# Kernel optimization log

Measured on AMD Instinct MI355X. Metric: run time of the kernel, lower is better.

The kernel has to match this reference:

```python
import jax, jax.numpy as jnp
import numpy as np

# Faithful RBF layer math:
# dists[n,k] = sum_d relu(sigma[d]) * (x[n,d]-center[k,d])^2  (original builds an NxN
# matrix per center just to take its diagonal; we use the algebraic expansion
# x^2.s - 2 (x*s).c^T + c^2.s which is O(N*K*D) and identical math)
# D2 = 1 - dists * relu(width); concat bias column of ones; out = D2_bias @ relu(W_out)

N, D, K, OUT = 131072, 256, 256, 128

def setup_inputs() -> dict:
    key = jax.random.key(0)
    k1, k2, k3, k4 = jax.random.split(key, 4)
    x = jax.random.normal(k1, (N, D), dtype=jnp.float32)
    # 'uniform' keras initializer ~ U(-0.05, 0.05)
    center = jax.random.uniform(k2, (K, D), minval=-0.05, maxval=0.05, dtype=jnp.float32)
    sigma = jax.random.uniform(k3, (1, D), minval=0.5, maxval=1.0, dtype=jnp.float32)
    width = jnp.ones((1, K), dtype=jnp.float32)
    output_weights = jax.random.uniform(k4, (1 + K, OUT), minval=0.5, maxval=1.0, dtype=jnp.float32)
    return {"x": x, "center": center, "sigma": sigma, "width": width,
            "output_weights": output_weights}

def reference(x, center, sigma, width, output_weights):
    s = jax.nn.relu(sigma[0])                       # [D]
    x2 = (x * x) @ s                                # [N]
    c2 = (center * center) @ s                      # [K]
    cross = (x * s) @ center.T                      # [N,K]
    dists = x2[:, None] - 2.0 * cross + c2[None, :] # [N,K] weighted sq-dists
    D2 = 1.0 - dists * jax.nn.relu(width)           # [N,K]
    ones = jnp.ones((x.shape[0], 1), dtype=x.dtype)
    D2_bias = jnp.concatenate([ones, D2], axis=1)   # [N,1+K]
    return D2_bias @ jax.nn.relu(output_weights)    # [N,OUT]
```

## Files before the change

### kernel.cpp

```cpp
#include <hip/hip_runtime.h>


typedef short  short8 __attribute__((ext_vector_type(8)));
typedef __bf16 bf16x8 __attribute__((ext_vector_type(8)));
typedef float  f32x4  __attribute__((ext_vector_type(4)));

#define N_ 131072
#define D_ 256
#define K_ 256
#define O_ 128

__device__ __forceinline__ unsigned short f2bf_bits(float f) {
  unsigned u = __builtin_bit_cast(unsigned, f);
  u += 0x7fffu + ((u >> 16) & 1u);
  return (unsigned short)(u >> 16);
}

__device__ __forceinline__ float relu(float v) { return v > 0.f ? v : 0.f; }

__global__ __launch_bounds__(256) void rbf_pre(
    const float* __restrict__ center, const float* __restrict__ sigma,
    const float* __restrict__ width,  const float* __restrict__ W,
    short* __restrict__ Mfrag, float* __restrict__ Bo, float* __restrict__ S1)
{
  const int tid = threadIdx.x;
  if (blockIdx.x < 64) {
    const int ot = blockIdx.x & 7;
    const int ks = blockIdx.x >> 3;
    __shared__ float ww[K_][16];
    __shared__ float cen[K_][32];
#pragma unroll
    for (int i = 0; i < 16; ++i) {
      const int k  = i * 16 + (tid >> 4);
      const int oc = tid & 15;
      ww[k][oc] = relu(width[k]) * relu(W[(1 + k) * O_ + ot * 16 + oc]);
    }
#pragma unroll
    for (int i = 0; i < 32; ++i) {
      const int k  = i * 8 + (tid >> 5);
      const int dc = tid & 31;
      cen[k][dc] = center[k * D_ + ks * 32 + dc];
    }
    __syncthreads();
    const int j   = tid & 7;
    const int lf  = tid >> 3;
    const int oc  = lf & 15;
    const int dc1 = (lf >> 4) * 8 + j;
    float a1 = 0.f, a2 = 0.f;
#pragma unroll 8
    for (int k = 0; k < K_; ++k) {
      const float w = ww[k][oc];
      a1 = fmaf(cen[k][dc1],      w, a1);
      a2 = fmaf(cen[k][dc1 + 16], w, a2);
    }
    const int e1 = blockIdx.x * 512 + tid;
    const int d1 = ks * 32 + dc1;
    Mfrag[e1]       = (short)f2bf_bits(a1 * relu(sigma[d1]));
    Mfrag[e1 + 256] = (short)f2bf_bits(a2 * relu(sigma[d1 + 16]));
  } else {
    __shared__ float c2s[K_];
    {
      const f32x4* cr = (const f32x4*)(center + tid * D_);
      const f32x4* sr = (const f32x4*)sigma;
      f32x4 acc = {0.f, 0.f, 0.f, 0.f};
#pragma unroll 8
      for (int d4 = 0; d4 < D_ / 4; ++d4) {
        const f32x4 c = cr[d4];
        const f32x4 s = sr[d4];
#pragma unroll
        for (int e = 0; e < 4; ++e) acc[e] = fmaf(c[e] * c[e], relu(s[e]), acc[e]);
      }
      c2s[tid] = (acc[0] + acc[1]) + (acc[2] + acc[3]);
    }
    __syncthreads();
    if (tid < O_) {
      const int o = tid;
      float s1 = 0.f, sum = 0.f, c2w = 0.f;
#pragma unroll 4
      for (int k = 0; k < K_; ++k) {
        const float w  = relu(width[k]);
        const float wr = relu(W[(1 + k) * O_ + o]);
        s1  = fmaf(w, wr, s1);
        sum += wr;
        c2w = fmaf(c2s[k] * w, wr, c2w);
      }
      Bo[o] = relu(W[o]) + sum - c2w;
      S1[o] = s1;
    }
  }
}

__global__ __launch_bounds__(512, 2) void rbf_main(
    const float* __restrict__ x, const float* __restrict__ sigma,
    const short* __restrict__ Mfrag, const float* __restrict__ Bo,
    const float* __restrict__ S1, float* __restrict__ out)
{
  __shared__ short8 Blds[4096];
  const int tid  = threadIdx.x;
  const int lane = tid & 63;
  const int wv   = tid >> 6;
  const int m    = lane & 15;
  const int q    = lane >> 4;
  const long rowBase = ((long)blockIdx.x * 8 + wv) * 16;

  short8 stg[8];
  const short8* Mf8 = (const short8*)Mfrag;
#pragma unroll
  for (int i = 0; i < 8; ++i) stg[i] = Mf8[i * 512 + tid];

  const float* xr = x + (rowBase + m) * D_ + q * 8;
  f32x4 raw[16];
#pragma unroll
  for (int ks = 0; ks < 8; ++ks) {
    raw[2 * ks]     = *(const f32x4*)(xr + ks * 32);
    raw[2 * ks + 1] = *(const f32x4*)(xr + ks * 32 + 4);
  }

#pragma unroll
  for (int i = 0; i < 8; ++i) Blds[i * 512 + tid] = stg[i];

  const float* sp = sigma + q * 8;
  bf16x8 a[8];
  float x2 = 0.f;
#pragma unroll
  for (int ks = 0; ks < 8; ++ks) {
    float sv[8], v[8];
    *(f32x4*)(sv)     = *(const f32x4*)(sp + ks * 32);
    *(f32x4*)(sv + 4) = *(const f32x4*)(sp + ks * 32 + 4);
    *(f32x4*)(v)      = raw[2 * ks];
    *(f32x4*)(v + 4)  = raw[2 * ks + 1];
    short8 ab;
#pragma unroll
    for (int jj = 0; jj < 8; ++jj) {
      const float s = relu(sv[jj]);
      x2 = fmaf(s * v[jj], v[jj], x2);
      ab[jj] = (short)f2bf_bits(v[jj]);
    }
    a[ks] = __builtin_bit_cast(bf16x8, ab);
  }
  x2 += __shfl_xor(x2, 16);
  x2 += __shfl_xor(x2, 32);

  __syncthreads();

#pragma unroll
  for (int ot = 0; ot < 8; ++ot) {
    f32x4 acc = {0.f, 0.f, 0.f, 0.f};
#pragma unroll
    for (int ks = 0; ks < 8; ++ks) {
      const bf16x8 bb =
          __builtin_bit_cast(bf16x8, Blds[(ks * 8 + ot) * 64 + lane]);
      acc = __builtin_amdgcn_mfma_f32_16x16x32_bf16(a[ks], bb, acc, 0, 0, 0);
    }
    const int   o  = ot * 16 + m;
    const float bo = Bo[o];
    const float s1 = S1[o];
    float* op = out + rowBase * O_ + o;
#pragma unroll
    for (int r = 0; r < 4; ++r) {
      const int rr = q * 4 + r;
      const float x2r = __shfl(x2, rr);
      op[(long)rr * O_] = fmaf(2.f, acc[r], fmaf(-x2r, s1, bo));
    }
  }
}

extern "C" void kernel_launch(void* const* d_in, const int* in_sizes, int n_in,
                              void* d_out, int out_size, void* d_ws, size_t ws_size,
                              hipStream_t stream) {
  (void)in_sizes; (void)n_in; (void)out_size; (void)ws_size;
  const float* x      = (const float*)d_in[0];
  const float* center = (const float*)d_in[1];
  const float* sigma  = (const float*)d_in[2];
  const float* width  = (const float*)d_in[3];
  const float* W      = (const float*)d_in[4];
  float* out = (float*)d_out;

  short* Mfrag = (short*)d_ws;
  float* Bo    = (float*)((char*)d_ws + 65536);
  float* S1    = (float*)((char*)d_ws + 66048);

  hipLaunchKernelGGL(rbf_pre, dim3(65), dim3(256), 0, stream,
                     center, sigma, width, W, Mfrag, Bo, S1);
  hipLaunchKernelGGL(rbf_main, dim3(1024), dim3(512), 0, stream,
                     x, sigma, Mfrag, Bo, S1, out);
}
```

Baseline: 249.3 us.

## Permute output columns for vectorized stores, async LDS load, higher occupancy

Permutes the output-column order inside the precomputed weight fragments so each lane owns four contiguous output columns. This lets the epilogue write with 16-byte vector stores instead of scalar strided stores. The B-fragment staging now uses global_load_lds to copy straight into LDS, bypassing registers. The MFMA loop is reordered to keep all eight accumulators live, the bias/S1 loads are hoisted and vectorized, and launch bounds are raised to four blocks per SM, which risks register pressure with eight accumulators plus the A fragments.

```diff
diff --git a/kernel.cpp b/kernel.cpp
--- a/kernel.cpp
+++ b/kernel.cpp
@@ -29,11 +29,12 @@
     const int ks = blockIdx.x >> 3;
     __shared__ float ww[K_][16];
     __shared__ float cen[K_][32];
+    const int ocol = (ot >> 2) * 64 + (tid & 15) * 4 + (ot & 3);
 #pragma unroll
     for (int i = 0; i < 16; ++i) {
       const int k  = i * 16 + (tid >> 4);
       const int oc = tid & 15;
-      ww[k][oc] = relu(width[k]) * relu(W[(1 + k) * O_ + ot * 16 + oc]);
+      ww[k][oc] = relu(width[k]) * relu(W[(1 + k) * O_ + ocol]);
     }
 #pragma unroll
     for (int i = 0; i < 32; ++i) {
@@ -90,7 +91,7 @@
   }
 }
 
-__global__ __launch_bounds__(512, 2) void rbf_main(
+__global__ __launch_bounds__(512, 4) void rbf_main(
     const float* __restrict__ x, const float* __restrict__ sigma,
     const short* __restrict__ Mfrag, const float* __restrict__ Bo,
     const float* __restrict__ S1, float* __restrict__ out)
@@ -103,65 +104,80 @@
   const int q    = lane >> 4;
   const long rowBase = ((long)blockIdx.x * 8 + wv) * 16;
 
-  short8 stg[8];
-  const short8* Mf8 = (const short8*)Mfrag;
-#pragma unroll
-  for (int i = 0; i < 8; ++i) stg[i] = Mf8[i * 512 + tid];
+  {
+    const short8* gsrc = (const short8*)Mfrag + wv * 64 + lane;
+    short8* ldst = &Blds[wv * 64];
+#pragma unroll
+    for (int i = 0; i < 8; ++i) {
+      __builtin_amdgcn_global_load_lds(
+          (const __attribute__((address_space(1))) unsigned int*)(gsrc + i * 512),
+          (__attribute__((address_space(3))) unsigned int*)(ldst + i * 512),
+          16, 0, 0);
+    }
+  }
 
   const float* xr = x + (rowBase + m) * D_ + q * 8;
-  f32x4 raw[16];
-#pragma unroll
-  for (int ks = 0; ks < 8; ++ks) {
-    raw[2 * ks]     = *(const f32x4*)(xr + ks * 32);
-    raw[2 * ks + 1] = *(const f32x4*)(xr + ks * 32 + 4);
-  }
-
-#pragma unroll
-  for (int i = 0; i < 8; ++i) Blds[i * 512 + tid] = stg[i];
-
   const float* sp = sigma + q * 8;
   bf16x8 a[8];
   float x2 = 0.f;
 #pragma unroll
   for (int ks = 0; ks < 8; ++ks) {
-    float sv[8], v[8];
-    *(f32x4*)(sv)     = *(const f32x4*)(sp + ks * 32);
-    *(f32x4*)(sv + 4) = *(const f32x4*)(sp + ks * 32 + 4);
-    *(f32x4*)(v)      = raw[2 * ks];
-    *(f32x4*)(v + 4)  = raw[2 * ks + 1];
-    short8 ab;
-#pragma unroll
-    for (int jj = 0; jj < 8; ++jj) {
-      const float s = relu(sv[jj]);
-      x2 = fmaf(s * v[jj], v[jj], x2);
-      ab[jj] = (short)f2bf_bits(v[jj]);
-    }
-    a[ks] = __builtin_bit_cast(bf16x8, ab);
+    const f32x4 v0  = *(const f32x4*)(xr + ks * 32);
+    const f32x4 v1  = *(const f32x4*)(xr + ks * 32 + 4);
+    const f32x4 sv0 = *(const f32x4*)(sp + ks * 32);
+    const f32x4 sv1 = *(const f32x4*)(sp + ks * 32 + 4);
+    bf16x8 av;
+#pragma unroll
+    for (int e = 0; e < 4; ++e) {
+      const float sa = relu(sv0[e]);
+      const float sb = relu(sv1[e]);
+      x2 = fmaf(sa * v0[e], v0[e], x2);
+      x2 = fmaf(sb * v1[e], v1[e], x2);
+      av[e]     = (__bf16)v0[e];
+      av[e + 4] = (__bf16)v1[e];
+    }
+    a[ks] = av;
   }
   x2 += __shfl_xor(x2, 16);
   x2 += __shfl_xor(x2, 32);
+  float x2b[4];
+#pragma unroll
+  for (int r = 0; r < 4; ++r) x2b[r] = __shfl(x2, q * 4 + r);
+
+  const f32x4 bo0 = *(const f32x4*)(Bo + m * 4);
+  const f32x4 bo1 = *(const f32x4*)(Bo + 64 + m * 4);
+  const f32x4 s10 = *(const f32x4*)(S1 + m * 4);
+  const f32x4 s11 = *(const f32x4*)(S1 + 64 + m * 4);
+
+  f32x4 accs[8];
+#pragma unroll
+  for (int ot = 0; ot < 8; ++ot) accs[ot] = (f32x4){0.f, 0.f, 0.f, 0.f};
 
   __syncthreads();
 
 #pragma unroll
-  for (int ot = 0; ot < 8; ++ot) {
-    f32x4 acc = {0.f, 0.f, 0.f, 0.f};
-#pragma unroll
-    for (int ks = 0; ks < 8; ++ks) {
+  for (int ks = 0; ks < 8; ++ks) {
+    const bf16x8 aa = a[ks];
+#pragma unroll
+    for (int ot = 0; ot < 8; ++ot) {
       const bf16x8 bb =
           __builtin_bit_cast(bf16x8, Blds[(ks * 8 + ot) * 64 + lane]);
-      acc = __builtin_amdgcn_mfma_f32_16x16x32_bf16(a[ks], bb, acc, 0, 0, 0);
-    }
-    const int   o  = ot * 16 + m;
-    const float bo = Bo[o];
-    const float s1 = S1[o];
-    float* op = out + rowBase * O_ + o;
-#pragma unroll
-    for (int r = 0; r < 4; ++r) {
-      const int rr = q * 4 + r;
-      const float x2r = __shfl(x2, rr);
-      op[(long)rr * O_] = fmaf(2.f, acc[r], fmaf(-x2r, s1, bo));
-    }
+      accs[ot] = __builtin_amdgcn_mfma_f32_16x16x32_bf16(aa, bb, accs[ot], 0, 0, 0);
+    }
+  }
+
+  float* orow = out + (rowBase + q * 4) * (long)O_ + m * 4;
+#pragma unroll
+  for (int r = 0; r < 4; ++r) {
+    const float x2r = x2b[r];
+    f32x4 lo, hi;
+#pragma unroll
+    for (int j = 0; j < 4; ++j) {
+      lo[j] = fmaf(2.f, accs[j][r],     fmaf(-x2r, s10[j], bo0[j]));
+      hi[j] = fmaf(2.f, accs[j + 4][r], fmaf(-x2r, s11[j], bo1[j]));
+    }
+    *(f32x4*)(orow + (long)r * O_)      = lo;
+    *(f32x4*)(orow + (long)r * O_ + 64) = hi;
   }
 }
 
```

Result: no change. 249.3 us (-0.0%).
